# Optimization experiments

Measured on AMD Instinct MI355X. Metric: run time of the kernel, lower is better.

The kernel has to match this reference:

```python
import jax, jax.numpy as jnp
import numpy as np
from jax import lax

M_ROWS, N_COLS = 2048, 4096
ADMM_ITERS = 30
CG_ITERS = 15


def setup_inputs() -> dict:
    key = jax.random.key(0)
    ks = jax.random.split(key, 6)
    A = jax.random.normal(ks[0], (M_ROWS, N_COLS), dtype=jnp.float32) / np.sqrt(N_COLS)
    c = jax.random.normal(ks[1], (N_COLS, 1), dtype=jnp.float32)
    # finite box bounds with lb < ub (isinf mask path in the original is vacuous here)
    lb = -(jnp.abs(jax.random.normal(ks[2], (M_ROWS, 1), dtype=jnp.float32)) + 0.1)
    ub = jnp.abs(jax.random.normal(ks[3], (M_ROWS, 1), dtype=jnp.float32)) + 0.1
    # positive diagonal scalings from the LP preconditioning (Ruiz-style)
    d = 0.5 + jax.random.uniform(ks[4], (N_COLS, 1), dtype=jnp.float32)
    e = 0.5 + jax.random.uniform(ks[5], (M_ROWS, 1), dtype=jnp.float32)
    return {
        "A": A, "c": c, "lb": lb, "ub": ub, "d": d, "e": e,
        "gamma_c": jnp.ones((1,), jnp.float32),   # gamma_c_mul * gamma_c
        "gamma_b": jnp.ones((1,), jnp.float32),   # gamma_b_mul * gamma_b
        "rho": jnp.ones((1,), jnp.float32),
        "sigma": jnp.full((1,), 1e-6, jnp.float32),  # exp(sigma_log), sigma_log=log(1e-6)
        "alpha": jnp.full((1,), 1.6, jnp.float32),
    }


def _pcg(matvec, b, Minv, x0, iters):
    """Fixed-iteration preconditioned conjugate gradient for SPD matvec."""
    r0 = b - matvec(x0)
    z0 = Minv(r0)
    rz0 = jnp.vdot(r0, z0)

    def body(carry, _):
        x, r, p, rz = carry
        Kp = matvec(p)
        a = rz / jnp.vdot(p, Kp)
        x = x + a * p
        r = r - a * Kp
        zv = Minv(r)
        rz_new = jnp.vdot(r, zv)
        p = zv + (rz_new / rz) * p
        return (x, r, p, rz_new), None

    (x, _, _, _), _ = lax.scan(body, (x0, r0, z0, rz0), None, length=iters)
    return x


def _admm_lp(A, c, lb, ub, d, e, gamma_c, gamma_b, rho, sigma, alpha):
    gc, gb = gamma_c[0], gamma_b[0]
    rho_s, sig_s, al_s = rho[0], sigma[0], alpha[0]
    m, n = A.shape

    c_s = gc * (d * c)                 # (n,1) scaled cost
    lb_s = gb * e * lb                 # (m,1)
    ub_s = gb * e * ub                 # (m,1)

    # diagonal preconditioner M = sigma + rho * ||A_:,j||^2
    Acnorm2 = jnp.sum(A * A, axis=0)[:, None]      # (n,1)
    Mdiag = sig_s + rho_s * Acnorm2
    Minv = lambda v: v / Mdiag
    Kop = lambda v: rho_s * (A.T @ (A @ v)) + sig_s * v

    x0 = jnp.zeros((n, 1), A.dtype)
    z0 = jnp.zeros((m, 1), A.dtype)
    y0 = jnp.zeros((m, 1), A.dtype)
    xt0 = jnp.zeros((n, 1), A.dtype)

    def step(carry, _):
        x, z, y, xtilde = carry
        right = sig_s * x - c_s + A.T @ (rho_s * z - y)
        xtilde = _pcg(Kop, right, Minv, xtilde, CG_ITERS)
        ztilde = A @ xtilde
        x = al_s * xtilde + (1.0 - al_s) * x
        ztilde = al_s * ztilde + (1.0 - al_s) * z
        z = jnp.clip(ztilde + y / rho_s, lb_s, ub_s)
        y = y + rho_s * (ztilde - z)
        return (x, z, y, xtilde), None

    (x, z, y, xtilde), _ = lax.scan(step, (x0, z0, y0, xt0), None, length=ADMM_ITERS)
    return x * d / gb                   # unscaled LP solution (n,1)


def reference(A, c, lb, ub, d, e, gamma_c, gamma_b, rho, sigma, alpha):
    return _admm_lp(A, c, lb, ub, d, e, gamma_c, gamma_b, rho, sigma, alpha)
```

## Files before the change

kernel.cpp:

```cpp
#include <hip/hip_runtime.h>

#define NWG 256
#define NT  512
#define ROWS 8
#define JPT 8
#define CPW 16
#define RPT 64
#define NDIM 4096
#define MROWS 2048
#define N_ADMM 30
#define N_CG 15

typedef unsigned long long ull;
typedef float f32x4 __attribute__((ext_vector_type(4)));

static_assert(NWG * ROWS == MROWS, "row partition");
static_assert(NT * JPT == NDIM, "col partition");
static_assert(NWG * CPW == NDIM, "col-slice partition");
static_assert(32 * RPT == MROWS, "col-slice rows");

__device__ __forceinline__ float wred64(float v) {
#pragma unroll
  for (int m = 32; m > 0; m >>= 1) v += __shfl_xor(v, m, 64);
  return v;
}
__device__ __forceinline__ float wred16(float v) {
  v += __shfl_xor(v, 1, 64); v += __shfl_xor(v, 2, 64);
  v += __shfl_xor(v, 4, 64); v += __shfl_xor(v, 8, 64);
  return v;
}
__device__ __forceinline__ void st64(ull* p, ull v) {
  __hip_atomic_store(p, v, __ATOMIC_RELAXED, __HIP_MEMORY_SCOPE_AGENT);
}
__device__ __forceinline__ ull ld64(const ull* p) {
  return __hip_atomic_load(p, __ATOMIC_RELAXED, __HIP_MEMORY_SCOPE_AGENT);
}
__device__ __forceinline__ f32x4 ntf4(const float* p) {
  return __builtin_nontemporal_load((const f32x4*)p);
}
__device__ __forceinline__ ull pk2(float a, float b) {
  return ((ull)__float_as_uint(b) << 32) | (ull)__float_as_uint(a);
}

__global__ __launch_bounds__(NT, 2)
void admm_lp_kernel(const float* __restrict__ A, const float* __restrict__ cvec,
                    const float* __restrict__ lbv, const float* __restrict__ ubv,
                    const float* __restrict__ dvec, const float* __restrict__ evec,
                    const float* __restrict__ gcp, const float* __restrict__ gbp,
                    const float* __restrict__ rhop, const float* __restrict__ sigp,
                    const float* __restrict__ alp,
                    float* __restrict__ out, unsigned char* __restrict__ ws)
{
  const int tid = threadIdx.x;
  const int w = blockIdx.x;
  const int j0 = tid * JPT;
  const int row0 = w * ROWS;
  const int g = tid >> 4;
  const int l = tid & 15;

  unsigned* kill  = (unsigned*)(ws + 128);
  ull* flags      = (ull*)(ws + 4096);
  float* z_g  = (float*)(ws + 32768);
  float* xt_g = (float*)(ws + 32768 + 16384);
  float* t_g  = (float*)(ws + 65536);
  float* u_g  = (float*)(ws + 65536 + 8192);
  ull* z64  = (ull*)z_g;
  ull* xt64 = (ull*)xt_g;
  ull* t64  = (ull*)t_g;
  ull* u64  = (ull*)u_g;

  __shared__ float s_scal[6];
  __shared__ float s_b[1];
  __shared__ float dred[8][ROWS];
  __shared__ float zb[ROWS], yb[ROWS], lbs[ROWS], ubs[ROWS];
  __shared__ float xa[16], cs[16], Md[16], r_l[16], pchunk[16], xtl[16];
  __shared__ float sredA[32][16], sredB[32][16];
  __shared__ int s_dead;

  float areg[ROWS][JPT];
  float acol[RPT];
  float preg[JPT];

  unsigned gen = 0;

  auto arrive_wait = [&](float partial) -> float {
    ++gen;
    __syncthreads();
    if (tid < 64 && !s_dead) {
      if (tid == 0) {
        __builtin_amdgcn_sched_barrier(0);
        asm volatile("s_waitcnt vmcnt(0)" ::: "memory");
        __builtin_amdgcn_sched_barrier(0);
        st64(&flags[(size_t)w * 8], ((ull)gen << 32) | (ull)__float_as_uint(partial));
      }
      ull* f0 = &flags[(size_t)(tid * 4 + 0) * 8];
      ull* f1 = &flags[(size_t)(tid * 4 + 1) * 8];
      ull* f2 = &flags[(size_t)(tid * 4 + 2) * 8];
      ull* f3 = &flags[(size_t)(tid * 4 + 3) * 8];
      ull v0, v1, v2, v3;
      int spin = 0;
      for (;;) {
        v0 = ld64(f0); v1 = ld64(f1); v2 = ld64(f2); v3 = ld64(f3);
        bool ok = ((unsigned)(v0 >> 32) >= gen) && ((unsigned)(v1 >> 32) >= gen) &&
                  ((unsigned)(v2 >> 32) >= gen) && ((unsigned)(v3 >> 32) >= gen);
        if (__all(ok)) break;
        __builtin_amdgcn_s_sleep(1);
        if ((++spin & 127) == 0) {
          if (__hip_atomic_load(kill, __ATOMIC_RELAXED, __HIP_MEMORY_SCOPE_AGENT) != 0u ||
              spin > 400000) {
            if (tid == 0) {
              s_dead = 1;
              __hip_atomic_store(kill, 1u, __ATOMIC_RELAXED, __HIP_MEMORY_SCOPE_AGENT);
            }
            break;
          }
        }
      }
      __builtin_amdgcn_sched_barrier(0);
      float s = __uint_as_float((unsigned)(v0 & 0xffffffffu))
              + __uint_as_float((unsigned)(v1 & 0xffffffffu))
              + __uint_as_float((unsigned)(v2 & 0xffffffffu))
              + __uint_as_float((unsigned)(v3 & 0xffffffffu));
      s = wred64(s);
      if (tid == 0) s_b[0] = s;
    }
    __syncthreads();
    return s_b[0];
  };

  if (tid == 0) {
    s_scal[0] = sigp[0]; s_scal[1] = rhop[0]; s_scal[2] = alp[0];
    s_scal[3] = gcp[0];  s_scal[4] = gbp[0];
    s_dead = 0;
  }
  {
#pragma unroll
    for (int r = 0; r < ROWS; ++r) {
      const float* ap = A + (size_t)(row0 + r) * NDIM + j0;
      const float4 a0 = *(const float4*)(ap);
      const float4 a1 = *(const float4*)(ap + 4);
      areg[r][0] = a0.x; areg[r][1] = a0.y; areg[r][2] = a0.z; areg[r][3] = a0.w;
      areg[r][4] = a1.x; areg[r][5] = a1.y; areg[r][6] = a1.z; areg[r][7] = a1.w;
    }
    float cn = 0.f;
#pragma unroll
    for (int r = 0; r < RPT; ++r) {
      acol[r] = A[(size_t)(g * RPT + r) * NDIM + w * CPW + l];
      cn += acol[r] * acol[r];
    }
    sredA[g][l] = cn;
  }
  __syncthreads();
  if (tid < ROWS) {
    const float gb = s_scal[4];
    zb[tid] = 0.f; yb[tid] = 0.f;
    const float ee = evec[row0 + tid];
    lbs[tid] = gb * ee * lbv[row0 + tid];
    ubs[tid] = gb * ee * ubv[row0 + tid];
  }
  const float sig = s_scal[0], rho = s_scal[1], al = s_scal[2];
  float rz_cur, rz_old = 1.f;
  {
    float zv = 0.f, apart = 0.f;
    if (tid < 16) {
      xa[tid] = 0.f; xtl[tid] = 0.f;
      cs[tid] = s_scal[3] * dvec[w * 16 + tid] * cvec[w * 16 + tid];
      float S = 0.f;
#pragma unroll
      for (int q = 0; q < 32; ++q) S += sredA[q][tid];
      Md[tid] = sig + rho * S;
      const float r0 = -cs[tid];
      r_l[tid] = r0;
      zv = r0 / Md[tid];
      float rzv = wred16(r0 * zv);
      if (tid == 0) apart = rzv;
    }
    if (tid < 64) {
      float a0 = __shfl(zv, (tid & 7) * 2, 64);
      float b0 = __shfl(zv, (tid & 7) * 2 + 1, 64);
      if (tid < 8) st64(&z64[(size_t)w * 8 + tid], pk2(a0, b0));
    }
    rz_cur = arrive_wait(apart);
  }

  for (int admm = 0; admm < N_ADMM; ++admm) {
    for (int cg = 0; cg < N_CG; ++cg) {
      float pkp_sum;
      {
        const float beta = (cg == 0) ? 0.f : (rz_cur / rz_old);
        rz_old = rz_cur;
        const f32x4 za = ntf4(z_g + j0);
        const f32x4 zc = ntf4(z_g + j0 + 4);
        float zl[JPT] = {za.x, za.y, za.z, za.w, zc.x, zc.y, zc.z, zc.w};
        if (cg == 0) {
#pragma unroll
          for (int k = 0; k < JPT; ++k) preg[k] = zl[k];
        } else {
#pragma unroll
          for (int k = 0; k < JPT; ++k) preg[k] = zl[k] + beta * preg[k];
        }
        if ((tid >> 1) == w) {
          const int b = (tid & 1) * JPT;
#pragma unroll
          for (int k = 0; k < JPT; ++k) pchunk[b + k] = preg[k];
        }
        float dp[ROWS];
#pragma unroll
        for (int r = 0; r < ROWS; ++r) {
          float s = 0.f;
#pragma unroll
          for (int k = 0; k < JPT; ++k) s += areg[r][k] * preg[k];
          dp[r] = s;
        }
#pragma unroll
        for (int r = 0; r < ROWS; ++r) {
          const float t = wred64(dp[r]);
          if ((tid & 63) == 0) dred[tid >> 6][r] = t;
        }
        __syncthreads();
        float srow = 0.f;
        if (tid < ROWS) {
          float s = 0.f;
#pragma unroll
          for (int q = 0; q < 8; ++q) s += dred[q][tid];
          srow = s;
        }
        float apart = 0.f;
        if (tid < 64) {
          float st2 = srow * srow;
          st2 += __shfl_xor(st2, 1, 64);
          st2 += __shfl_xor(st2, 2, 64);
          st2 += __shfl_xor(st2, 4, 64);
          float a0 = __shfl(srow, (tid & 3) * 2, 64);
          float b0 = __shfl(srow, (tid & 3) * 2 + 1, 64);
          if (tid < 4) st64(&t64[(size_t)w * 4 + tid], pk2(a0, b0));
          if (tid == 0) {
            float sp = 0.f;
#pragma unroll
            for (int li = 0; li < 16; ++li) sp += pchunk[li] * pchunk[li];
            apart = rho * st2 + sig * sp;
          }
        }
        pkp_sum = arrive_wait(apart);
      }
      {
        const float a = rz_old / pkp_sum;
        float part = 0.f;
#pragma unroll
        for (int r4 = 0; r4 < RPT / 4; ++r4) {
          const f32x4 tv = ntf4(t_g + g * RPT + r4 * 4);
          part += tv.x * acol[r4 * 4 + 0] + tv.y * acol[r4 * 4 + 1]
                + tv.z * acol[r4 * 4 + 2] + tv.w * acol[r4 * 4 + 3];
        }
        sredA[g][l] = part;
        __syncthreads();
        float zzv = 0.f, xtv = 0.f, apart = 0.f;
        if (tid < 16) {
          float S = 0.f;
#pragma unroll
          for (int q = 0; q < 32; ++q) S += sredA[q][tid];
          const float Kp = rho * S + sig * pchunk[tid];
          const float rn = r_l[tid] - a * Kp;
          r_l[tid] = rn;
          xtl[tid] += a * pchunk[tid];
          xtv = xtl[tid];
          zzv = rn / Md[tid];
          float rzv = wred16(rn * zzv);
          if (tid == 0) apart = rzv;
        }
        if (tid < 64) {
          float a0 = __shfl(zzv, (tid & 7) * 2, 64);
          float b0 = __shfl(zzv, (tid & 7) * 2 + 1, 64);
          if (tid < 8) st64(&z64[(size_t)w * 8 + tid], pk2(a0, b0));
          if (cg == N_CG - 1) {
            float c0 = __shfl(xtv, (tid & 7) * 2, 64);
            float d0 = __shfl(xtv, (tid & 7) * 2 + 1, 64);
            if (tid < 8) st64(&xt64[(size_t)w * 8 + tid], pk2(c0, d0));
          }
        }
        rz_cur = arrive_wait(apart);
      }
    }
    if (admm < N_ADMM - 1) {
      {
        const f32x4 xv0 = ntf4(xt_g + j0);
        const f32x4 xv1 = ntf4(xt_g + j0 + 4);
        float xl[JPT] = {xv0.x, xv0.y, xv0.z, xv0.w, xv1.x, xv1.y, xv1.z, xv1.w};
        float dp[ROWS];
#pragma unroll
        for (int r = 0; r < ROWS; ++r) {
          float s = 0.f;
#pragma unroll
          for (int k = 0; k < JPT; ++k) s += areg[r][k] * xl[k];
          dp[r] = s;
        }
#pragma unroll
        for (int r = 0; r < ROWS; ++r) {
          const float t = wred64(dp[r]);
          if ((tid & 63) == 0) dred[tid >> 6][r] = t;
        }
        __syncthreads();
        float srow = 0.f, urow = 0.f;
        if (tid < ROWS) {
          float s = 0.f;
#pragma unroll
          for (int q = 0; q < 8; ++q) s += dred[q][tid];
          srow = s;
          const float zt = al * s + (1.f - al) * zb[tid];
          float zn = zt + yb[tid] / rho;
          zn = fminf(fmaxf(zn, lbs[tid]), ubs[tid]);
          const float yn = yb[tid] + rho * (zt - zn);
          zb[tid] = zn; yb[tid] = yn;
          urow = rho * zn - yn;
        }
        if (tid < 64) {
          float ta = __shfl(srow, (tid & 3) * 2, 64);
          float tb = __shfl(srow, (tid & 3) * 2 + 1, 64);
          float ua = __shfl(urow, (tid & 3) * 2, 64);
          float ub = __shfl(urow, (tid & 3) * 2 + 1, 64);
          if (tid < 4) {
            st64(&t64[(size_t)w * 4 + tid], pk2(ta, tb));
            st64(&u64[(size_t)w * 4 + tid], pk2(ua, ub));
          }
        }
        if ((tid >> 1) == w) {
          const int b = (tid & 1) * JPT;
#pragma unroll
          for (int k = 0; k < JPT; ++k) xa[b + k] = al * xl[k] + (1.f - al) * xa[b + k];
        }
        (void)arrive_wait(0.f);
      }
      {
        float pk = 0.f, pr = 0.f;
#pragma unroll
        for (int r4 = 0; r4 < RPT / 4; ++r4) {
          const f32x4 tv = ntf4(t_g + g * RPT + r4 * 4);
          const f32x4 uv = ntf4(u_g + g * RPT + r4 * 4);
          pk += tv.x * acol[r4 * 4 + 0] + tv.y * acol[r4 * 4 + 1]
              + tv.z * acol[r4 * 4 + 2] + tv.w * acol[r4 * 4 + 3];
          pr += uv.x * acol[r4 * 4 + 0] + uv.y * acol[r4 * 4 + 1]
              + uv.z * acol[r4 * 4 + 2] + uv.w * acol[r4 * 4 + 3];
        }
        sredA[g][l] = pk; sredB[g][l] = pr;
        __syncthreads();
        float zv = 0.f, apart = 0.f;
        if (tid < 16) {
          float SK = 0.f, SR = 0.f;
#pragma unroll
          for (int q = 0; q < 32; ++q) { SK += sredA[q][tid]; SR += sredB[q][tid]; }
          const float right = sig * xa[tid] - cs[tid] + SR;
          const float Kx = rho * SK + sig * xtl[tid];
          const float r0 = right - Kx;
          r_l[tid] = r0;
          zv = r0 / Md[tid];
          float rzv = wred16(r0 * zv);
          if (tid == 0) apart = rzv;
        }
        if (tid < 64) {
          float a0 = __shfl(zv, (tid & 7) * 2, 64);
          float b0 = __shfl(zv, (tid & 7) * 2 + 1, 64);
          if (tid < 8) st64(&z64[(size_t)w * 8 + tid], pk2(a0, b0));
        }
        rz_cur = arrive_wait(apart);
      }
    }
  }
  if (tid < 16) {
    const float gb = s_scal[4];
    const float xf = al * xtl[tid] + (1.f - al) * xa[tid];
    out[w * 16 + tid] = xf * dvec[w * 16 + tid] / gb;
  }
}

extern "C" void kernel_launch(void* const* d_in, const int* in_sizes, int n_in,
                              void* d_out, int out_size, void* d_ws, size_t ws_size,
                              hipStream_t stream) {
  const float* A   = (const float*)d_in[0];
  const float* c   = (const float*)d_in[1];
  const float* lb  = (const float*)d_in[2];
  const float* ub  = (const float*)d_in[3];
  const float* dv  = (const float*)d_in[4];
  const float* ev  = (const float*)d_in[5];
  const float* gc  = (const float*)d_in[6];
  const float* gb  = (const float*)d_in[7];
  const float* rho = (const float*)d_in[8];
  const float* sg  = (const float*)d_in[9];
  const float* al  = (const float*)d_in[10];
  float* out = (float*)d_out;
  unsigned char* ws = (unsigned char*)d_ws;

  (void)hipMemsetAsync(d_ws, 0, 1u << 15, stream);

  admm_lp_kernel<<<dim3(NWG), dim3(NT), 0, stream>>>(
      A, c, lb, ub, dv, ev, gc, gb, rho, sg, al, out, ws);
}
```

Measured before the change: 5.195 ms.

## Split grid barrier into producer-wait and wave0 reduction with double-buffered flags

Replaces the monolithic arrive/wait grid barrier with a publish step, a per-wave wait on producer flags in alternating flag banks, and a wave-0-only poll that also sums the partial scalars. The CG recurrence is rewritten so that the search direction is carried through the A*p row sums (t = Az + beta*t), which removes the per-thread p register array and moves the scalar bookkeeping into wave-0 registers instead of shared memory. The aim is to drop a __syncthreads and the shared-memory broadcast from each global synchronisation. The trade-off is more subtle ordering assumptions across the double-buffered flags and a reformulated recurrence that may accumulate rounding differently.

```diff
diff --git a/kernel.cpp b/kernel.cpp
--- a/kernel.cpp
+++ b/kernel.cpp
@@ -24,7 +24,11 @@
   for (int m = 32; m > 0; m >>= 1) v += __shfl_xor(v, m, 64);
   return v;
 }
-__device__ __forceinline__ float wred16(float v) {
+__device__ __forceinline__ float sum8(float v) {
+  v += __shfl_xor(v, 1, 64); v += __shfl_xor(v, 2, 64); v += __shfl_xor(v, 4, 64);
+  return v;
+}
+__device__ __forceinline__ float sum16(float v) {
   v += __shfl_xor(v, 1, 64); v += __shfl_xor(v, 2, 64);
   v += __shfl_xor(v, 4, 64); v += __shfl_xor(v, 8, 64);
   return v;
@@ -41,6 +45,14 @@
 __device__ __forceinline__ ull pk2(float a, float b) {
   return ((ull)__float_as_uint(b) << 32) | (ull)__float_as_uint(a);
 }
+
+#define WS_KILL   128
+#define WS_BANK0  8192
+#define WS_BANK1  24576
+#define WS_Z      49152
+#define WS_XT     65536
+#define WS_T      81920
+#define WS_U      90112
 
 __global__ __launch_bounds__(NT, 2)
 void admm_lp_kernel(const float* __restrict__ A, const float* __restrict__ cvec,
@@ -53,79 +65,93 @@
 {
   const int tid = threadIdx.x;
   const int w = blockIdx.x;
+  const int wv = tid >> 6;
+  const int lane = tid & 63;
   const int j0 = tid * JPT;
   const int row0 = w * ROWS;
   const int g = tid >> 4;
   const int l = tid & 15;
 
-  unsigned* kill  = (unsigned*)(ws + 128);
-  ull* flags      = (ull*)(ws + 4096);
-  float* z_g  = (float*)(ws + 32768);
-  float* xt_g = (float*)(ws + 32768 + 16384);
-  float* t_g  = (float*)(ws + 65536);
-  float* u_g  = (float*)(ws + 65536 + 8192);
-  ull* z64  = (ull*)z_g;
-  ull* xt64 = (ull*)xt_g;
-  ull* t64  = (ull*)t_g;
-  ull* u64  = (ull*)u_g;
+  unsigned* kill = (unsigned*)(ws + WS_KILL);
+  ull* fbank[2] = { (ull*)(ws + WS_BANK0), (ull*)(ws + WS_BANK1) };
+  float* z_g  = (float*)(ws + WS_Z);
+  float* xt_g = (float*)(ws + WS_XT);
+  float* t_g  = (float*)(ws + WS_T);
+  float* u_g  = (float*)(ws + WS_U);
+  ull* z64 = (ull*)z_g; ull* xt64 = (ull*)xt_g; ull* t64 = (ull*)t_g; ull* u64 = (ull*)u_g;
 
   __shared__ float s_scal[6];
-  __shared__ float s_b[1];
   __shared__ float dred[8][ROWS];
-  __shared__ float zb[ROWS], yb[ROWS], lbs[ROWS], ubs[ROWS];
-  __shared__ float xa[16], cs[16], Md[16], r_l[16], pchunk[16], xtl[16];
-  __shared__ float sredA[32][16], sredB[32][16];
+  __shared__ float sredA[32][16];
+  __shared__ float sredB[32][16];
   __shared__ int s_dead;
 
   float areg[ROWS][JPT];
   float acol[RPT];
-  float preg[JPT];
 
   unsigned gen = 0;
 
-  auto arrive_wait = [&](float partial) -> float {
-    ++gen;
-    __syncthreads();
-    if (tid < 64 && !s_dead) {
-      if (tid == 0) {
-        __builtin_amdgcn_sched_barrier(0);
-        asm volatile("s_waitcnt vmcnt(0)" ::: "memory");
-        __builtin_amdgcn_sched_barrier(0);
-        st64(&flags[(size_t)w * 8], ((ull)gen << 32) | (ull)__float_as_uint(partial));
-      }
-      ull* f0 = &flags[(size_t)(tid * 4 + 0) * 8];
-      ull* f1 = &flags[(size_t)(tid * 4 + 1) * 8];
-      ull* f2 = &flags[(size_t)(tid * 4 + 2) * 8];
-      ull* f3 = &flags[(size_t)(tid * 4 + 3) * 8];
-      ull v0, v1, v2, v3;
+  auto wait_prod = [&](unsigned G) {
+    if (s_dead) return;
+    ull* fp = &fbank[G & 1][(size_t)(wv * 32 + (lane & 31)) * 8];
+    int spin = 0;
+    for (;;) {
+      ull v = ld64(fp);
+      if (__all((unsigned)(v >> 32) >= G)) break;
+      __builtin_amdgcn_s_sleep(1);
+      if ((++spin & 127) == 0) {
+        if (__hip_atomic_load(kill, __ATOMIC_RELAXED, __HIP_MEMORY_SCOPE_AGENT) != 0u ||
+            spin > 300000) {
+          s_dead = 1;
+          __hip_atomic_store(kill, 1u, __ATOMIC_RELAXED, __HIP_MEMORY_SCOPE_AGENT);
+          break;
+        }
+      }
+    }
+    asm volatile("" ::: "memory");
+    __builtin_amdgcn_sched_barrier(0);
+  };
+
+  auto poll_all = [&](unsigned G) -> float {
+    ull v0 = 0, v1 = 0, v2 = 0, v3 = 0;
+    if (!s_dead) {
+      ull* fb = fbank[G & 1];
+      ull* f0 = &fb[(size_t)(lane * 4 + 0) * 8];
+      ull* f1 = &fb[(size_t)(lane * 4 + 1) * 8];
+      ull* f2 = &fb[(size_t)(lane * 4 + 2) * 8];
+      ull* f3 = &fb[(size_t)(lane * 4 + 3) * 8];
       int spin = 0;
       for (;;) {
         v0 = ld64(f0); v1 = ld64(f1); v2 = ld64(f2); v3 = ld64(f3);
-        bool ok = ((unsigned)(v0 >> 32) >= gen) && ((unsigned)(v1 >> 32) >= gen) &&
-                  ((unsigned)(v2 >> 32) >= gen) && ((unsigned)(v3 >> 32) >= gen);
+        bool ok = ((unsigned)(v0 >> 32) >= G) && ((unsigned)(v1 >> 32) >= G) &&
+                  ((unsigned)(v2 >> 32) >= G) && ((unsigned)(v3 >> 32) >= G);
         if (__all(ok)) break;
         __builtin_amdgcn_s_sleep(1);
         if ((++spin & 127) == 0) {
           if (__hip_atomic_load(kill, __ATOMIC_RELAXED, __HIP_MEMORY_SCOPE_AGENT) != 0u ||
-              spin > 400000) {
-            if (tid == 0) {
-              s_dead = 1;
-              __hip_atomic_store(kill, 1u, __ATOMIC_RELAXED, __HIP_MEMORY_SCOPE_AGENT);
-            }
+              spin > 300000) {
+            s_dead = 1;
+            __hip_atomic_store(kill, 1u, __ATOMIC_RELAXED, __HIP_MEMORY_SCOPE_AGENT);
             break;
           }
         }
       }
-      __builtin_amdgcn_sched_barrier(0);
-      float s = __uint_as_float((unsigned)(v0 & 0xffffffffu))
-              + __uint_as_float((unsigned)(v1 & 0xffffffffu))
-              + __uint_as_float((unsigned)(v2 & 0xffffffffu))
-              + __uint_as_float((unsigned)(v3 & 0xffffffffu));
-      s = wred64(s);
-      if (tid == 0) s_b[0] = s;
-    }
-    __syncthreads();
-    return s_b[0];
+    }
+    asm volatile("" ::: "memory");
+    __builtin_amdgcn_sched_barrier(0);
+    float s = __uint_as_float((unsigned)(v0 & 0xffffffffu))
+            + __uint_as_float((unsigned)(v1 & 0xffffffffu))
+            + __uint_as_float((unsigned)(v2 & 0xffffffffu))
+            + __uint_as_float((unsigned)(v3 & 0xffffffffu));
+    return wred64(s);
+  };
+
+  auto publish = [&](float partial) {
+    asm volatile("s_waitcnt vmcnt(0)" ::: "memory");
+    __builtin_amdgcn_sched_barrier(0);
+    if (lane == 0 && !s_dead)
+      st64(&fbank[(gen + 1) & 1][(size_t)w * 8],
+           ((ull)(gen + 1) << 32) | (ull)__float_as_uint(partial));
   };
 
   if (tid == 0) {
@@ -151,141 +177,127 @@
     sredA[g][l] = cn;
   }
   __syncthreads();
-  if (tid < ROWS) {
-    const float gb = s_scal[4];
-    zb[tid] = 0.f; yb[tid] = 0.f;
-    const float ee = evec[row0 + tid];
-    lbs[tid] = gb * ee * lbv[row0 + tid];
-    ubs[tid] = gb * ee * ubv[row0 + tid];
+
+  const float sig = s_scal[0], rho = s_scal[1], al = s_scal[2];
+
+  float f_cs = 0.f, f_Md = 1.f, f_rl = 0.f, f_pch = 0.f, f_xtl = 0.f, f_xa = 0.f;
+  float f_zown = 0.f, f_trow = 0.f, f_zb = 0.f, f_yb = 0.f, f_lbs = 0.f, f_ubs = 0.f;
+  float rz_cur = 1.f, gbv = 1.f;
+
+  if (wv == 0) {
+    gbv = s_scal[4];
+    if (lane < 8) {
+      const float ee = evec[row0 + lane];
+      f_lbs = gbv * ee * lbv[row0 + lane];
+      f_ubs = gbv * ee * ubv[row0 + lane];
+    }
+    if (lane < 16) {
+      f_cs = s_scal[3] * dvec[w * 16 + lane] * cvec[w * 16 + lane];
+      float S = 0.f;
+#pragma unroll
+      for (int q = 0; q < 32; ++q) S += sredA[q][lane];
+      f_Md = sig + rho * S;
+      f_rl = -f_cs;
+      f_zown = f_rl / f_Md;
+    }
+    float rzp = (lane < 16) ? f_rl * f_zown : 0.f;
+    rzp = sum16(rzp);
+    float a0 = __shfl(f_zown, (lane & 7) * 2, 64);
+    float b0 = __shfl(f_zown, (lane & 7) * 2 + 1, 64);
+    if (lane < 8) st64(&z64[(size_t)w * 8 + lane], pk2(a0, b0));
+    publish(rzp);
   }
-  const float sig = s_scal[0], rho = s_scal[1], al = s_scal[2];
-  float rz_cur, rz_old = 1.f;
-  {
-    float zv = 0.f, apart = 0.f;
-    if (tid < 16) {
-      xa[tid] = 0.f; xtl[tid] = 0.f;
-      cs[tid] = s_scal[3] * dvec[w * 16 + tid] * cvec[w * 16 + tid];
-      float S = 0.f;
-#pragma unroll
-      for (int q = 0; q < 32; ++q) S += sredA[q][tid];
-      Md[tid] = sig + rho * S;
-      const float r0 = -cs[tid];
-      r_l[tid] = r0;
-      zv = r0 / Md[tid];
-      float rzv = wred16(r0 * zv);
-      if (tid == 0) apart = rzv;
-    }
-    if (tid < 64) {
-      float a0 = __shfl(zv, (tid & 7) * 2, 64);
-      float b0 = __shfl(zv, (tid & 7) * 2 + 1, 64);
-      if (tid < 8) st64(&z64[(size_t)w * 8 + tid], pk2(a0, b0));
-    }
-    rz_cur = arrive_wait(apart);
-  }
+  ++gen;
 
   for (int admm = 0; admm < N_ADMM; ++admm) {
     for (int cg = 0; cg < N_CG; ++cg) {
-      float pkp_sum;
       {
-        const float beta = (cg == 0) ? 0.f : (rz_cur / rz_old);
-        rz_old = rz_cur;
+        wait_prod(gen);
         const f32x4 za = ntf4(z_g + j0);
         const f32x4 zc = ntf4(z_g + j0 + 4);
-        float zl[JPT] = {za.x, za.y, za.z, za.w, zc.x, zc.y, zc.z, zc.w};
-        if (cg == 0) {
-#pragma unroll
-          for (int k = 0; k < JPT; ++k) preg[k] = zl[k];
-        } else {
-#pragma unroll
-          for (int k = 0; k < JPT; ++k) preg[k] = zl[k] + beta * preg[k];
-        }
-        if ((tid >> 1) == w) {
-          const int b = (tid & 1) * JPT;
-#pragma unroll
-          for (int k = 0; k < JPT; ++k) pchunk[b + k] = preg[k];
-        }
+        const float zl[JPT] = {za.x, za.y, za.z, za.w, zc.x, zc.y, zc.z, zc.w};
         float dp[ROWS];
 #pragma unroll
         for (int r = 0; r < ROWS; ++r) {
           float s = 0.f;
 #pragma unroll
-          for (int k = 0; k < JPT; ++k) s += areg[r][k] * preg[k];
+          for (int k = 0; k < JPT; ++k) s += areg[r][k] * zl[k];
           dp[r] = s;
         }
 #pragma unroll
         for (int r = 0; r < ROWS; ++r) {
           const float t = wred64(dp[r]);
-          if ((tid & 63) == 0) dred[tid >> 6][r] = t;
+          if (lane == 0) dred[wv][r] = t;
         }
         __syncthreads();
-        float srow = 0.f;
-        if (tid < ROWS) {
-          float s = 0.f;
-#pragma unroll
-          for (int q = 0; q < 8; ++q) s += dred[q][tid];
-          srow = s;
-        }
-        float apart = 0.f;
-        if (tid < 64) {
-          float st2 = srow * srow;
-          st2 += __shfl_xor(st2, 1, 64);
-          st2 += __shfl_xor(st2, 2, 64);
-          st2 += __shfl_xor(st2, 4, 64);
-          float a0 = __shfl(srow, (tid & 3) * 2, 64);
-          float b0 = __shfl(srow, (tid & 3) * 2 + 1, 64);
-          if (tid < 4) st64(&t64[(size_t)w * 4 + tid], pk2(a0, b0));
-          if (tid == 0) {
-            float sp = 0.f;
-#pragma unroll
-            for (int li = 0; li < 16; ++li) sp += pchunk[li] * pchunk[li];
-            apart = rho * st2 + sig * sp;
-          }
-        }
-        pkp_sum = arrive_wait(apart);
+        if (wv == 0) {
+          const float rz_new = poll_all(gen);
+          const float beta = (cg == 0) ? 0.f : rz_new / rz_cur;
+          rz_cur = rz_new;
+          float az = 0.f;
+          if (lane < 8) {
+#pragma unroll
+            for (int q = 0; q < 8; ++q) az += dred[q][lane];
+          }
+          f_trow = az + beta * f_trow;
+          f_pch  = f_zown + beta * f_pch;
+          float st2 = (lane < 8) ? f_trow * f_trow : 0.f;
+          st2 = sum8(st2);
+          float sp2 = (lane < 16) ? f_pch * f_pch : 0.f;
+          sp2 = sum16(sp2);
+          const float part = rho * st2 + sig * sp2;
+          float a0 = __shfl(f_trow, (lane & 3) * 2, 64);
+          float b0 = __shfl(f_trow, (lane & 3) * 2 + 1, 64);
+          if (lane < 4) st64(&t64[(size_t)w * 4 + lane], pk2(a0, b0));
+          publish(part);
+        }
+        ++gen;
       }
       {
-        const float a = rz_old / pkp_sum;
-        float part = 0.f;
+        wait_prod(gen);
+        float up = 0.f;
 #pragma unroll
         for (int r4 = 0; r4 < RPT / 4; ++r4) {
           const f32x4 tv = ntf4(t_g + g * RPT + r4 * 4);
-          part += tv.x * acol[r4 * 4 + 0] + tv.y * acol[r4 * 4 + 1]
-                + tv.z * acol[r4 * 4 + 2] + tv.w * acol[r4 * 4 + 3];
-        }
-        sredA[g][l] = part;
+          up += tv.x * acol[r4 * 4 + 0] + tv.y * acol[r4 * 4 + 1]
+              + tv.z * acol[r4 * 4 + 2] + tv.w * acol[r4 * 4 + 3];
+        }
+        sredA[g][l] = up;
         __syncthreads();
-        float zzv = 0.f, xtv = 0.f, apart = 0.f;
-        if (tid < 16) {
+        if (wv == 0) {
+          const float pkp = poll_all(gen);
+          const float alpha = rz_cur / pkp;
           float S = 0.f;
-#pragma unroll
-          for (int q = 0; q < 32; ++q) S += sredA[q][tid];
-          const float Kp = rho * S + sig * pchunk[tid];
-          const float rn = r_l[tid] - a * Kp;
-          r_l[tid] = rn;
-          xtl[tid] += a * pchunk[tid];
-          xtv = xtl[tid];
-          zzv = rn / Md[tid];
-          float rzv = wred16(rn * zzv);
-          if (tid == 0) apart = rzv;
-        }
-        if (tid < 64) {
-          float a0 = __shfl(zzv, (tid & 7) * 2, 64);
-          float b0 = __shfl(zzv, (tid & 7) * 2 + 1, 64);
-          if (tid < 8) st64(&z64[(size_t)w * 8 + tid], pk2(a0, b0));
+          if (lane < 16) {
+#pragma unroll
+            for (int q = 0; q < 32; ++q) S += sredA[q][lane];
+          }
+          const float Kp = rho * S + sig * f_pch;
+          const float rn = f_rl - alpha * Kp;
+          f_rl = rn;
+          f_xtl += alpha * f_pch;
+          f_zown = rn / f_Md;
+          float rzp = (lane < 16) ? rn * f_zown : 0.f;
+          rzp = sum16(rzp);
+          float a0 = __shfl(f_zown, (lane & 7) * 2, 64);
+          float b0 = __shfl(f_zown, (lane & 7) * 2 + 1, 64);
+          if (lane < 8) st64(&z64[(size_t)w * 8 + lane], pk2(a0, b0));
           if (cg == N_CG - 1) {
-            float c0 = __shfl(xtv, (tid & 7) * 2, 64);
-            float d0 = __shfl(xtv, (tid & 7) * 2 + 1, 64);
-            if (tid < 8) st64(&xt64[(size_t)w * 8 + tid], pk2(c0, d0));
-          }
-        }
-        rz_cur = arrive_wait(apart);
+            float c0 = __shfl(f_xtl, (lane & 7) * 2, 64);
+            float d0 = __shfl(f_xtl, (lane & 7) * 2 + 1, 64);
+            if (lane < 8) st64(&xt64[(size_t)w * 8 + lane], pk2(c0, d0));
+          }
+          publish(rzp);
+        }
+        ++gen;
       }
     }
     if (admm < N_ADMM - 1) {
       {
+        wait_prod(gen);
         const f32x4 xv0 = ntf4(xt_g + j0);
         const f32x4 xv1 = ntf4(xt_g + j0 + 4);
-        float xl[JPT] = {xv0.x, xv0.y, xv0.z, xv0.w, xv1.x, xv1.y, xv1.z, xv1.w};
+        const float xl[JPT] = {xv0.x, xv0.y, xv0.z, xv0.w, xv1.x, xv1.y, xv1.z, xv1.w};
         float dp[ROWS];
 #pragma unroll
         for (int r = 0; r < ROWS; ++r) {
@@ -297,40 +309,36 @@
 #pragma unroll
         for (int r = 0; r < ROWS; ++r) {
           const float t = wred64(dp[r]);
-          if ((tid & 63) == 0) dred[tid >> 6][r] = t;
+          if (lane == 0) dred[wv][r] = t;
         }
         __syncthreads();
-        float srow = 0.f, urow = 0.f;
-        if (tid < ROWS) {
-          float s = 0.f;
-#pragma unroll
-          for (int q = 0; q < 8; ++q) s += dred[q][tid];
-          srow = s;
-          const float zt = al * s + (1.f - al) * zb[tid];
-          float zn = zt + yb[tid] / rho;
-          zn = fminf(fmaxf(zn, lbs[tid]), ubs[tid]);
-          const float yn = yb[tid] + rho * (zt - zn);
-          zb[tid] = zn; yb[tid] = yn;
-          urow = rho * zn - yn;
-        }
-        if (tid < 64) {
-          float ta = __shfl(srow, (tid & 3) * 2, 64);
-          float tb = __shfl(srow, (tid & 3) * 2 + 1, 64);
-          float ua = __shfl(urow, (tid & 3) * 2, 64);
-          float ub = __shfl(urow, (tid & 3) * 2 + 1, 64);
-          if (tid < 4) {
-            st64(&t64[(size_t)w * 4 + tid], pk2(ta, tb));
-            st64(&u64[(size_t)w * 4 + tid], pk2(ua, ub));
-          }
-        }
-        if ((tid >> 1) == w) {
-          const int b = (tid & 1) * JPT;
-#pragma unroll
-          for (int k = 0; k < JPT; ++k) xa[b + k] = al * xl[k] + (1.f - al) * xa[b + k];
-        }
-        (void)arrive_wait(0.f);
+        if (wv == 0) {
+          (void)poll_all(gen);
+          float ztr = 0.f, urow = 0.f;
+          if (lane < 8) {
+#pragma unroll
+            for (int q = 0; q < 8; ++q) ztr += dred[q][lane];
+            const float zt = al * ztr + (1.f - al) * f_zb;
+            float zn = fminf(fmaxf(zt + f_yb / rho, f_lbs), f_ubs);
+            const float yn = f_yb + rho * (zt - zn);
+            f_zb = zn; f_yb = yn;
+            urow = rho * zn - yn;
+          }
+          f_xa = al * f_xtl + (1.f - al) * f_xa;
+          float ta = __shfl(ztr,  (lane & 3) * 2, 64);
+          float tb = __shfl(ztr,  (lane & 3) * 2 + 1, 64);
+          float ua = __shfl(urow, (lane & 3) * 2, 64);
+          float ub = __shfl(urow, (lane & 3) * 2 + 1, 64);
+          if (lane < 4) {
+            st64(&t64[(size_t)w * 4 + lane], pk2(ta, tb));
+            st64(&u64[(size_t)w * 4 + lane], pk2(ua, ub));
+          }
+          publish(0.f);
+        }
+        ++gen;
       }
       {
+        wait_prod(gen);
         float pk = 0.f, pr = 0.f;
 #pragma unroll
         for (int r4 = 0; r4 < RPT / 4; ++r4) {
@@ -343,32 +351,32 @@
         }
         sredA[g][l] = pk; sredB[g][l] = pr;
         __syncthreads();
-        float zv = 0.f, apart = 0.f;
-        if (tid < 16) {
+        if (wv == 0) {
+          (void)poll_all(gen);
           float SK = 0.f, SR = 0.f;
-#pragma unroll
-          for (int q = 0; q < 32; ++q) { SK += sredA[q][tid]; SR += sredB[q][tid]; }
-          const float right = sig * xa[tid] - cs[tid] + SR;
-          const float Kx = rho * SK + sig * xtl[tid];
+          if (lane < 16) {
+#pragma unroll
+            for (int q = 0; q < 32; ++q) { SK += sredA[q][lane]; SR += sredB[q][lane]; }
+          }
+          const float right = sig * f_xa - f_cs + SR;
+          const float Kx = rho * SK + sig * f_xtl;
           const float r0 = right - Kx;
-          r_l[tid] = r0;
-          zv = r0 / Md[tid];
-          float rzv = wred16(r0 * zv);
-          if (tid == 0) apart = rzv;
-        }
-        if (tid < 64) {
-          float a0 = __shfl(zv, (tid & 7) * 2, 64);
-          float b0 = __shfl(zv, (tid & 7) * 2 + 1, 64);
-          if (tid < 8) st64(&z64[(size_t)w * 8 + tid], pk2(a0, b0));
-        }
-        rz_cur = arrive_wait(apart);
+          f_rl = r0;
+          f_zown = r0 / f_Md;
+          float rzp = (lane < 16) ? r0 * f_zown : 0.f;
+          rzp = sum16(rzp);
+          float a0 = __shfl(f_zown, (lane & 7) * 2, 64);
+          float b0 = __shfl(f_zown, (lane & 7) * 2 + 1, 64);
+          if (lane < 8) st64(&z64[(size_t)w * 8 + lane], pk2(a0, b0));
+          publish(rzp);
+        }
+        ++gen;
       }
     }
   }
-  if (tid < 16) {
-    const float gb = s_scal[4];
-    const float xf = al * xtl[tid] + (1.f - al) * xa[tid];
-    out[w * 16 + tid] = xf * dvec[w * 16 + tid] / gb;
+  if (wv == 0 && lane < 16) {
+    const float xf = al * f_xtl + (1.f - al) * f_xa;
+    out[w * 16 + lane] = xf * dvec[w * 16 + lane] / gbv;
   }
 }
 
@@ -389,7 +397,7 @@
   float* out = (float*)d_out;
   unsigned char* ws = (unsigned char*)d_ws;
 
-  (void)hipMemsetAsync(d_ws, 0, 1u << 15, stream);
+  (void)hipMemsetAsync(d_ws, 0, 40960, stream);
 
   admm_lp_kernel<<<dim3(NWG), dim3(NT), 0, stream>>>(
       A, c, lb, ub, dv, ev, gc, gb, rho, sg, al, out, ws);
```

Measured after the change: 5.776 ms. 1.11x slower.
